# Optimization experiments

Hardware: AMD Instinct MI355X
Metric: run time of the kernel (lower is better)

## Reference

```python
import jax, jax.numpy as jnp
import numpy as np

B, S, H = 8, 1024, 1024
NH, HD = 16, 64  # num heads, head dim


def _split_heads(x):
    # [B,S,H] -> [B,NH,S,HD]
    return x.reshape(B, S, NH, HD).transpose(0, 2, 1, 3)


def setup_inputs() -> dict:
    key = jax.random.key(0)
    ks = jax.random.split(key, 16)
    sc = 1.0 / np.sqrt(H)
    sch = 1.0 / np.sqrt(HD)
    return {
        "hidden_states": jax.random.normal(ks[0], (B, S, H), jnp.float32),
        "attention_mask": jnp.zeros((B, 1, 1, S), jnp.float32),
        "context_embedded": jax.random.normal(ks[1], (B, S, H), jnp.float32),
        "Wq": jax.random.normal(ks[2], (H, H), jnp.float32) * sc,
        "bq": jnp.zeros((H,), jnp.float32),
        "Wk": jax.random.normal(ks[3], (H, H), jnp.float32) * sc,
        "bk": jnp.zeros((H,), jnp.float32),
        "Wv": jax.random.normal(ks[4], (H, H), jnp.float32) * sc,
        "bv": jnp.zeros((H,), jnp.float32),
        "Wcq": jax.random.normal(ks[5], (HD, HD), jnp.float32) * sch,
        "bcq": jnp.zeros((HD,), jnp.float32),
        "Wck": jax.random.normal(ks[6], (HD, HD), jnp.float32) * sch,
        "bck": jnp.zeros((HD,), jnp.float32),
        "w_lqc": jax.random.normal(ks[7], (HD,), jnp.float32) * sch,
        "w_lqq": jax.random.normal(ks[8], (HD,), jnp.float32) * sch,
        "w_lkc": jax.random.normal(ks[9], (HD,), jnp.float32) * sch,
        "w_lkk": jax.random.normal(ks[10], (HD,), jnp.float32) * sch,
    }


def reference(hidden_states, attention_mask, context_embedded,
              Wq, bq, Wk, bk, Wv, bv, Wcq, bcq, Wck, bck,
              w_lqc, w_lqq, w_lkc, w_lkk):
    # projections -> [B,NH,S,HD]
    q = _split_heads(hidden_states @ Wq + bq)
    k = _split_heads(hidden_states @ Wk + bk)
    v = _split_heads(hidden_states @ Wv + bv)
    ce = _split_heads(context_embedded)

    # context gating for queries
    ce_q = ce @ Wcq + bcq
    lam_q = jax.nn.sigmoid(ce_q @ w_lqc[:, None] + q @ w_lqq[:, None])  # [B,NH,S,1]
    q_ctx = (1.0 - lam_q) * q + lam_q * ce_q

    # context gating for keys
    ce_k = ce @ Wck + bck
    lam_k = jax.nn.sigmoid(ce_k @ w_lkc[:, None] + k @ w_lkk[:, None])  # [B,NH,S,1]
    k_ctx = (1.0 - lam_k) * k + lam_k * ce_k

    scores = jnp.einsum("bhqd,bhkd->bhqk", q_ctx, k_ctx) / np.sqrt(HD)
    scores = scores + attention_mask
    probs = jax.nn.softmax(scores, axis=-1)
    ctx = jnp.einsum("bhqk,bhkd->bhqd", probs, v)
    return ctx.transpose(0, 2, 1, 3).reshape(B, S, H)
```

## Files before the change

kernel.cpp:

```cpp
#include <hip/hip_runtime.h>

typedef _Float16 f16;
typedef f16   f16x8 __attribute__((ext_vector_type(8)));
typedef float f32x4 __attribute__((ext_vector_type(4)));

namespace {
constexpr int kB  = 8;
constexpr int kS  = 1024;
constexpr int kH  = 1024;
constexpr int kNH = 16;
constexpr int kHD = 64;
constexpr int kBH = kB * kNH;
constexpr int kRows = kBH * kS;
}

__device__ __forceinline__ void async16(const f16* g, f16* l) {
    __builtin_amdgcn_global_load_lds(
        (const __attribute__((address_space(1))) unsigned int*)g,
        (__attribute__((address_space(3))) unsigned int*)l, 16, 0, 0);
}

__device__ __forceinline__ int phys4(int m, int c) {
    return ((m >> 1) << 3) | ((((m & 1) << 2) | c) ^ ((m >> 1) & 7));
}
__device__ __forceinline__ int phys8(int m, int c) {
    return (m << 3) | (c ^ (m & 7));
}

__global__ __launch_bounds__(256) void cast_inputs_kernel(
    const float* __restrict__ hs, const float* __restrict__ ce,
    f16* __restrict__ hs16, f16* __restrict__ ce16)
{
    int i = (blockIdx.x * 256 + threadIdx.x) * 8;
    const float* src = blockIdx.y ? ce : hs;
    float4 a = *(const float4*)(src + i);
    float4 b = *(const float4*)(src + i + 4);
    union { f16 h[8]; uint4 u; } pk;
    pk.h[0] = (f16)a.x; pk.h[1] = (f16)a.y; pk.h[2] = (f16)a.z; pk.h[3] = (f16)a.w;
    pk.h[4] = (f16)b.x; pk.h[5] = (f16)b.y; pk.h[6] = (f16)b.z; pk.h[7] = (f16)b.w;
    if (blockIdx.y == 0) {
        *(uint4*)(hs16 + i) = pk.u;
    } else {
        int row = i >> 10, col = i & 1023;
        int bb = row >> 10, s = row & 1023;
        int h = col >> 6, d = col & 63;
        size_t o = ((((size_t)(bb * kNH + h) << 10) | s) << 6) | d;
        *(uint4*)(ce16 + o) = pk.u;
    }
}

__global__ __launch_bounds__(256) void transpose_w_kernel(
    const float* __restrict__ Wq, const float* __restrict__ Wk,
    const float* __restrict__ Wv, f16* __restrict__ Wt)
{
    const float* W = (blockIdx.z == 0) ? Wq : (blockIdx.z == 1) ? Wk : Wv;
    f16* out = Wt + (size_t)blockIdx.z * kH * kH;
    __shared__ f16 T[64][72];
    const int tid = threadIdx.x;
    const int k0 = blockIdx.y * 64, n0 = blockIdx.x * 64;
#pragma unroll
    for (int i = 0; i < 4; ++i) {
        int idx = tid + i * 256;
        int r = idx >> 4, cb = (idx & 15) * 4;
        float4 v = *(const float4*)(W + (size_t)(k0 + r) * kH + n0 + cb);
        T[cb + 0][r] = (f16)v.x; T[cb + 1][r] = (f16)v.y;
        T[cb + 2][r] = (f16)v.z; T[cb + 3][r] = (f16)v.w;
    }
    __syncthreads();
#pragma unroll
    for (int i = 0; i < 4; ++i) {
        int idx = tid + i * 256;
        int r = idx >> 4, cb = (idx & 15) * 4;
        union { f16 h[4]; uint2 u; } pk;
#pragma unroll
        for (int j = 0; j < 4; ++j) pk.h[j] = T[r][cb + j];
        *(uint2*)(out + (size_t)(n0 + r) * kH + k0 + cb) = pk.u;
    }
}

__global__ __launch_bounds__(256) void transpose_wc_kernel(
    const float* __restrict__ Wcq, const float* __restrict__ Wck,
    f16* __restrict__ Wct)
{
    const float* W = blockIdx.x ? Wck : Wcq;
    f16* out = Wct + blockIdx.x * kHD * kHD;
    const int t = threadIdx.x;
#pragma unroll
    for (int i = 0; i < 16; ++i) {
        int idx = i * 256 + t;
        int k = idx >> 6, n = idx & 63;
        out[n * 64 + k] = (f16)W[idx];
    }
}

__global__ __launch_bounds__(256) void maskmax_kernel(
    const float* __restrict__ mask, float* __restrict__ mm)
{
    const int b = blockIdx.x, t = threadIdx.x;
    const float* mp = mask + b * kS;
    float v = fmaxf(fmaxf(mp[t], mp[t + 256]), fmaxf(mp[t + 512], mp[t + 768]));
#pragma unroll
    for (int off = 1; off < 64; off <<= 1) v = fmaxf(v, __shfl_xor(v, off, 64));
    __shared__ float red[4];
    if ((t & 63) == 0) red[t >> 6] = v;
    __syncthreads();
    if (t == 0) mm[b] = fmaxf(fmaxf(red[0], red[1]), fmaxf(red[2], red[3]));
}

__global__ __launch_bounds__(256) void qkv_gemm_f16(
    const f16* __restrict__ hs16, const f16* __restrict__ Wt,
    const float* __restrict__ bq, const float* __restrict__ bk,
    const float* __restrict__ bv,
    f16* __restrict__ q16, f16* __restrict__ k16, f16* __restrict__ vt)
{
    const int z = blockIdx.z;
    const f16* Bmat = Wt + (size_t)z * kH * kH;
    const float* bias = (z == 0) ? bq : (z == 1) ? bk : bv;

    __shared__ f16 Atile[128 * 32];
    __shared__ f16 Btile[128 * 32];
    __shared__ f16 Cb[4][64 * 20];

    const int tid = threadIdx.x;
    const int w = tid >> 6, lane = tid & 63;
    const int quad = lane >> 4, mh = lane & 15;
    const int wm = w >> 1, wn = w & 1;
    const int m0 = blockIdx.x * 128, n0 = blockIdx.y * 128;

    const f16* aptr[2]; const f16* bptr[2];
#pragma unroll
    for (int i = 0; i < 2; ++i) {
        int P = (w * 2 + i) * 64 + lane;
        int r2 = P >> 3, s = P & 7;
        int bb = s ^ (r2 & 7);
        int m = (r2 << 1) | (bb >> 2), c = bb & 3;
        aptr[i] = hs16 + (size_t)(m0 + m) * kH + c * 8;
        bptr[i] = Bmat + (size_t)(n0 + m) * kH + c * 8;
    }

    f32x4 acc[4][4];
#pragma unroll
    for (int i = 0; i < 4; ++i)
#pragma unroll
        for (int j = 0; j < 4; ++j) acc[i][j] = (f32x4){0.f, 0.f, 0.f, 0.f};

    int aoff[4], boff[4];
#pragma unroll
    for (int t = 0; t < 4; ++t) {
        aoff[t] = phys4(wm * 64 + t * 16 + mh, quad) * 8;
        boff[t] = phys4(wn * 64 + t * 16 + mh, quad) * 8;
    }

    for (int kt = 0; kt < 32; ++kt) {
        __syncthreads();
        async16(aptr[0], Atile + (w * 2 + 0) * 512);
        async16(aptr[1], Atile + (w * 2 + 1) * 512);
        async16(bptr[0], Btile + (w * 2 + 0) * 512);
        async16(bptr[1], Btile + (w * 2 + 1) * 512);
        aptr[0] += 32; aptr[1] += 32; bptr[0] += 32; bptr[1] += 32;
        __syncthreads();

        f16x8 af[4], bf[4];
#pragma unroll
        for (int t = 0; t < 4; ++t) af[t] = *(const f16x8*)(Atile + aoff[t]);
#pragma unroll
        for (int t = 0; t < 4; ++t) bf[t] = *(const f16x8*)(Btile + boff[t]);
#pragma unroll
        for (int i = 0; i < 4; ++i)
#pragma unroll
            for (int j = 0; j < 4; ++j)
                acc[i][j] = __builtin_amdgcn_mfma_f32_16x16x32_f16(
                    af[i], bf[j], acc[i][j], 0, 0, 0);
    }

    if (z < 2) {
        f16* outp = (z == 0) ? q16 : k16;
        const int h    = (n0 + wn * 64) >> 6;
        const int bbb  = m0 >> 10;
        const int sb   = (m0 & 1023) + wm * 64;
        f16* base = outp + ((size_t)(bbb * kNH + h) * kS + sb) * kHD;
#pragma unroll
        for (int nt = 0; nt < 4; ++nt) {
            const float bn = bias[n0 + wn * 64 + nt * 16 + mh];
#pragma unroll
            for (int mt = 0; mt < 4; ++mt)
#pragma unroll
                for (int r = 0; r < 4; ++r)
                    Cb[w][(mt * 16 + quad * 4 + r) * 20 + mh] =
                        (f16)(acc[mt][nt][r] + bn);
#pragma unroll
            for (int p = 0; p < 4; ++p) {
                int row = (lane >> 2) + p * 16;
                int qtr = lane & 3;
                uint2 v = *(const uint2*)(&Cb[w][row * 20 + qtr * 4]);
                *(uint2*)(base + (size_t)row * kHD + nt * 16 + qtr * 4) = v;
            }
        }
    } else {
#pragma unroll
        for (int nt = 0; nt < 4; ++nt) {
            const int n = n0 + wn * 64 + nt * 16 + mh;
            const int h = n >> 6, d = n & 63;
            const float bn = bias[n];
#pragma unroll
            for (int mt = 0; mt < 4; ++mt) {
                int mbase = m0 + wm * 64 + mt * 16 + quad * 4;
                int bbb = mbase >> 10, s0 = mbase & 1023;
                union { f16 h4[4]; uint2 u; } pk;
#pragma unroll
                for (int r = 0; r < 4; ++r) pk.h4[r] = (f16)(acc[mt][nt][r] + bn);
                *(uint2*)(vt + ((size_t)(bbb * kNH + h) * kHD + d) * kS + s0) = pk.u;
            }
        }
    }
}

__global__ __launch_bounds__(256) void gate_mfma(
    const f16* __restrict__ ce16, const f16* __restrict__ Wct,
    const float* __restrict__ bcq, const float* __restrict__ bck,
    const float* __restrict__ wlqc, const float* __restrict__ wlqq,
    const float* __restrict__ wlkc, const float* __restrict__ wlkk,
    f16* __restrict__ q16, f16* __restrict__ k16,
    unsigned int* __restrict__ kn)
{
    __shared__ f16 Wls[64 * 64];
    __shared__ f16 CeQ[4][64 * 64];
    __shared__ float Tp[4][64 * 17];
    __shared__ float lamS[4][64];

    const int tid = threadIdx.x, w = tid >> 6, lane = tid & 63;
    const int quad = lane >> 4, mh = lane & 15;
    const int gate = blockIdx.x >> 9;
    const int tIdx = (blockIdx.x & 511) * 4 + w;
    const size_t row0 = (size_t)tIdx * 64;

    const float* bc  = gate ? bck  : bcq;
    const float* wlc = gate ? wlkc : wlqc;
    const float* wlx = gate ? wlkk : wlqq;
    f16* xw = (gate ? k16 : q16) + row0 * kHD;
    const f16* cep = ce16 + row0 * kHD;
    const f16* Wcg = Wct + gate * kHD * kHD;

#pragma unroll
    for (int i = 0; i < 2; ++i) {
        int P = tid + i * 256;
        int m = P >> 3, c = P & 7;
        *(uint4*)(Wls + phys8(m, c) * 8) = *(const uint4*)(Wcg + m * 64 + c * 8);
    }
#pragma unroll
    for (int i = 0; i < 8; ++i) {
        int P = i * 64 + lane;
        int m = P >> 3, c = (P & 7) ^ (m & 7);
        async16(cep + m * 64 + c * 8, CeQ[w] + i * 512);
    }
    __syncthreads();

#pragma unroll
    for (int it = 0; it < 8; ++it) {
        int slot = it * 64 + lane;
        int r = slot >> 3, c = slot & 7;
        union { uint4 u; f16 h[8]; } xv;
        xv.u = *(const uint4*)(xw + r * 64 + c * 8);
        float4 wa = ((const float4*)wlx)[c * 2];
        float4 wb = ((const float4*)wlx)[c * 2 + 1];
        float s = (float)xv.h[0] * wa.x + (float)xv.h[1] * wa.y +
                  (float)xv.h[2] * wa.z + (float)xv.h[3] * wa.w +
                  (float)xv.h[4] * wb.x + (float)xv.h[5] * wb.y +
                  (float)xv.h[6] * wb.z + (float)xv.h[7] * wb.w;
        s += __shfl_xor(s, 1, 64);
        s += __shfl_xor(s, 2, 64);
        s += __shfl_xor(s, 4, 64);
        if ((lane & 7) == 0) Tp[w][r * 17 + 16] = s;
    }

    f32x4 acc[4][4];
#pragma unroll
    for (int i = 0; i < 4; ++i)
#pragma unroll
        for (int j = 0; j < 4; ++j) acc[i][j] = (f32x4){0.f, 0.f, 0.f, 0.f};

    f16x8 bfr[4][2];
#pragma unroll
    for (int nt = 0; nt < 4; ++nt)
#pragma unroll
        for (int ks = 0; ks < 2; ++ks)
            bfr[nt][ks] = *(const f16x8*)(Wls + phys8(nt * 16 + mh, ks * 4 + quad) * 8);
#pragma unroll
    for (int mt = 0; mt < 4; ++mt) {
        f16x8 a0 = *(const f16x8*)(CeQ[w] + phys8(mt * 16 + mh, 0 + quad) * 8);
        f16x8 a1 = *(const f16x8*)(CeQ[w] + phys8(mt * 16 + mh, 4 + quad) * 8);
#pragma unroll
        for (int nt = 0; nt < 4; ++nt) {
            acc[mt][nt] = __builtin_amdgcn_mfma_f32_16x16x32_f16(a0, bfr[nt][0], acc[mt][nt], 0, 0, 0);
            acc[mt][nt] = __builtin_amdgcn_mfma_f32_16x16x32_f16(a1, bfr[nt][1], acc[mt][nt], 0, 0, 0);
        }
    }

    float bcv[4], wlcv[4];
#pragma unroll
    for (int nt = 0; nt < 4; ++nt) {
        int n = nt * 16 + mh;
        bcv[nt] = bc[n]; wlcv[nt] = wlc[n];
    }
#pragma unroll
    for (int mt = 0; mt < 4; ++mt) {
#pragma unroll
        for (int r = 0; r < 4; ++r) {
            int m = mt * 16 + quad * 4 + r;
            float tpv = 0.f;
#pragma unroll
            for (int nt = 0; nt < 4; ++nt) {
                float v = acc[mt][nt][r] + bcv[nt];
                int col = nt * 16 + mh;
                CeQ[w][phys8(m, col >> 3) * 8 + (col & 7)] = (f16)v;
                tpv += v * wlcv[nt];
            }
            Tp[w][m * 17 + mh] = tpv;
        }
    }

    float t = 0.f;
#pragma unroll
    for (int j = 0; j < 17; ++j) t += Tp[w][lane * 17 + j];
    lamS[w][lane] = 1.0f / (1.0f + __expf(-t));

    float wmax = 0.f;
#pragma unroll
    for (int it = 0; it < 8; ++it) {
        int slot = it * 64 + lane;
        int r = slot >> 3, c = slot & 7;
        float lam = lamS[w][r];
        union { uint4 u; f16 h[8]; } xv;
        xv.u = *(const uint4*)(xw + r * 64 + c * 8);
        f16x8 cq = *(const f16x8*)(CeQ[w] + phys8(r, c) * 8);
        union { f16 h[8]; uint4 u; } o;
        float ss = 0.f;
#pragma unroll
        for (int j = 0; j < 8; ++j) {
            o.h[j] = (f16)((1.0f - lam) * (float)xv.h[j] + lam * (float)cq[j]);
            float fv = (float)o.h[j];
            ss += fv * fv;
        }
        *(uint4*)(xw + r * 64 + c * 8) = o.u;
        if (gate) {
            ss += __shfl_xor(ss, 1, 64);
            ss += __shfl_xor(ss, 2, 64);
            ss += __shfl_xor(ss, 4, 64);
            wmax = fmaxf(wmax, ss);
        }
    }
    if (gate) {
        wmax = fmaxf(wmax, __shfl_xor(wmax, 8, 64));
        wmax = fmaxf(wmax, __shfl_xor(wmax, 16, 64));
        wmax = fmaxf(wmax, __shfl_xor(wmax, 32, 64));
        if (lane == 0) atomicMax(&kn[tIdx >> 4], __float_as_uint(wmax));
    }
}

__global__ __launch_bounds__(256) void attn_f16(
    const f16* __restrict__ q16, const f16* __restrict__ k16,
    const f16* __restrict__ vt, const float* __restrict__ mask,
    const unsigned int* __restrict__ kn, const float* __restrict__ mm,
    float* __restrict__ out)
{
    __shared__ f16 Ks[2][64 * 64];
    __shared__ f16 Vs[2][64 * 64];
    __shared__ f16 Ps[4][32 * 68];

    const int tid = threadIdx.x;
    const int w = tid >> 6, lane = tid & 63;
    const int quad = lane >> 4, mh = lane & 15;
    const int bh = blockIdx.x, bbb = bh >> 4, h = bh & 15;
    const int q0 = blockIdx.y * 128;
    const float* maskb = mask + bbb * kS;

    int mS[2], cS[2];
#pragma unroll
    for (int i = 0; i < 2; ++i) {
        int P = (w * 2 + i) * 64 + lane;
        mS[i] = P >> 3;
        cS[i] = (P & 7) ^ (mS[i] & 7);
    }
    const f16* kp[2]; const f16* vp[2];
#pragma unroll
    for (int i = 0; i < 2; ++i) {
        kp[i] = k16 + ((size_t)bh * kS + mS[i]) * kHD + cS[i] * 8;
        vp[i] = vt  + ((size_t)bh * kHD + mS[i]) * kS + cS[i] * 8;
    }

    auto issue = [&](f16* Kb, f16* Vb) {
#pragma unroll
        for (int i = 0; i < 2; ++i) {
            async16(kp[i], Kb + (w * 2 + i) * 512);
            async16(vp[i], Vb + (w * 2 + i) * 512);
            kp[i] += 64 * kHD;
            vp[i] += 64;
        }
    };

    issue(Ks[0], Vs[0]);

    f16x8 qf[2][2];
#pragma unroll
    for (int rt = 0; rt < 2; ++rt) {
        const f16* qrow = q16 + ((size_t)bh * kS + q0 + w * 32 + rt * 16 + mh) * kHD;
#pragma unroll
        for (int ks = 0; ks < 2; ++ks) {
            qf[rt][ks] = *(const f16x8*)(qrow + ks * 32 + quad * 8);
#pragma unroll
            for (int j = 0; j < 8; ++j) qf[rt][ks][j] *= (f16)0.125f;
        }
    }

    const float kn2 = __uint_as_float(kn[bh]);
    const float mmb = mm[bbb];
    float bndr[2][4];
#pragma unroll
    for (int rt = 0; rt < 2; ++rt) {
        float qn2 = 0.f;
#pragma unroll
        for (int ks = 0; ks < 2; ++ks)
#pragma unroll
            for (int j = 0; j < 8; ++j) {
                float v = (float)qf[rt][ks][j];
                qn2 += v * v;
            }
        qn2 += __shfl_xor(qn2, 16, 64);
        qn2 += __shfl_xor(qn2, 32, 64);
        const float bnd = sqrtf(qn2 * kn2) + mmb - 9.5f;
#pragma unroll
        for (int r = 0; r < 4; ++r) bndr[rt][r] = __shfl(bnd, quad * 4 + r, 64);
    }

    f32x4 O[2][4];
#pragma unroll
    for (int rt = 0; rt < 2; ++rt)
#pragma unroll
        for (int i = 0; i < 4; ++i) O[rt][i] = (f32x4){0.f, 0.f, 0.f, 0.f};
    float lsum[2][4] = {{0.f, 0.f, 0.f, 0.f}, {0.f, 0.f, 0.f, 0.f}};

    auto step = [&](const f16* Kb, const f16* Vb, int jt) {
        f32x4 S[2][4];
#pragma unroll
        for (int nt = 0; nt < 4; ++nt) {
            f16x8 kf0 = *(const f16x8*)(Kb + phys8(nt * 16 + mh, 0 + quad) * 8);
            f16x8 kf1 = *(const f16x8*)(Kb + phys8(nt * 16 + mh, 4 + quad) * 8);
#pragma unroll
            for (int rt = 0; rt < 2; ++rt) {
                S[rt][nt] = __builtin_amdgcn_mfma_f32_16x16x32_f16(
                    qf[rt][0], kf0, (f32x4){0.f, 0.f, 0.f, 0.f}, 0, 0, 0);
                S[rt][nt] = __builtin_amdgcn_mfma_f32_16x16x32_f16(
                    qf[rt][1], kf1, S[rt][nt], 0, 0, 0);
            }
        }
#pragma unroll
        for (int nt = 0; nt < 4; ++nt) {
            const float mv = maskb[jt + nt * 16 + mh];
#pragma unroll
            for (int rt = 0; rt < 2; ++rt)
#pragma unroll
                for (int r = 0; r < 4; ++r) {
                    float e = __expf(S[rt][nt][r] + mv - bndr[rt][r]);
                    lsum[rt][r] += e;
                    Ps[w][(rt * 16 + quad * 4 + r) * 68 + nt * 16 + mh] = (f16)e;
                }
        }
        f16x8 pf[2][2];
#pragma unroll
        for (int rt = 0; rt < 2; ++rt)
#pragma unroll
            for (int ks = 0; ks < 2; ++ks)
                pf[rt][ks] = *(const f16x8*)(
                    &Ps[w][(rt * 16 + mh) * 68 + ks * 32 + quad * 8]);
#pragma unroll
        for (int dt = 0; dt < 4; ++dt) {
            f16x8 vf0 = *(const f16x8*)(Vb + phys8(dt * 16 + mh, 0 + quad) * 8);
            f16x8 vf1 = *(const f16x8*)(Vb + phys8(dt * 16 + mh, 4 + quad) * 8);
#pragma unroll
            for (int rt = 0; rt < 2; ++rt) {
                O[rt][dt] = __builtin_amdgcn_mfma_f32_16x16x32_f16(
                    pf[rt][0], vf0, O[rt][dt], 0, 0, 0);
                O[rt][dt] = __builtin_amdgcn_mfma_f32_16x16x32_f16(
                    pf[rt][1], vf1, O[rt][dt], 0, 0, 0);
            }
        }
    };

    __syncthreads();

    for (int jt = 0; jt < kS; jt += 128) {
        issue(Ks[1], Vs[1]);
        step(Ks[0], Vs[0], jt);
        __syncthreads();
        if (jt + 128 < kS) issue(Ks[0], Vs[0]);
        step(Ks[1], Vs[1], jt + 64);
        __syncthreads();
    }

#pragma unroll
    for (int rt = 0; rt < 2; ++rt)
#pragma unroll
        for (int r = 0; r < 4; ++r) {
#pragma unroll
            for (int off = 1; off < 16; off <<= 1)
                lsum[rt][r] += __shfl_xor(lsum[rt][r], off, 64);
            lsum[rt][r] = 1.0f / lsum[rt][r];
        }
#pragma unroll
    for (int rt = 0; rt < 2; ++rt)
#pragma unroll
        for (int dt = 0; dt < 4; ++dt)
#pragma unroll
            for (int r = 0; r < 4; ++r) {
                const int s = q0 + w * 32 + rt * 16 + quad * 4 + r;
                out[((size_t)(bbb * kS + s)) * kH + (h << 6) + dt * 16 + mh] =
                    O[rt][dt][r] * lsum[rt][r];
            }
}

extern "C" void kernel_launch(void* const* d_in, const int* in_sizes, int n_in,
                              void* d_out, int out_size, void* d_ws, size_t ws_size,
                              hipStream_t stream) {
    (void)in_sizes; (void)n_in; (void)out_size; (void)ws_size;

    const float* hs   = (const float*)d_in[0];
    const float* mask = (const float*)d_in[1];
    const float* ce   = (const float*)d_in[2];
    const float* Wq   = (const float*)d_in[3];
    const float* bq   = (const float*)d_in[4];
    const float* Wk   = (const float*)d_in[5];
    const float* bk   = (const float*)d_in[6];
    const float* Wv   = (const float*)d_in[7];
    const float* bv   = (const float*)d_in[8];
    const float* Wcq  = (const float*)d_in[9];
    const float* bcq  = (const float*)d_in[10];
    const float* Wck  = (const float*)d_in[11];
    const float* bck  = (const float*)d_in[12];
    const float* wlqc = (const float*)d_in[13];
    const float* wlqq = (const float*)d_in[14];
    const float* wlkc = (const float*)d_in[15];
    const float* wlkk = (const float*)d_in[16];
    float* out = (float*)d_out;

    f16* hs16 = (f16*)d_ws;
    f16* Wt   = hs16 + (size_t)kB * kS * kH;
    f16* q16  = Wt + (size_t)3 * kH * kH;
    f16* k16  = q16 + (size_t)kRows * kHD;
    f16* vt   = k16 + (size_t)kRows * kHD;
    f16* ce16 = vt + (size_t)kRows * kHD;
    f16* Wct  = ce16 + (size_t)kRows * kHD;
    unsigned int* kn = (unsigned int*)(Wct + 2 * kHD * kHD);
    float* mm = (float*)(kn + kBH);

    hipMemsetAsync(kn, 0, kBH * sizeof(unsigned int), stream);

    cast_inputs_kernel<<<dim3(kB * kS * kH / (256 * 8), 2), 256, 0, stream>>>(
        hs, ce, hs16, ce16);
    transpose_w_kernel<<<dim3(16, 16, 3), 256, 0, stream>>>(Wq, Wk, Wv, Wt);
    transpose_wc_kernel<<<dim3(2), 256, 0, stream>>>(Wcq, Wck, Wct);
    maskmax_kernel<<<dim3(kB), 256, 0, stream>>>(mask, mm);

    qkv_gemm_f16<<<dim3(kB * kS / 128, kH / 128, 3), 256, 0, stream>>>(
        hs16, Wt, bq, bk, bv, q16, k16, vt);

    gate_mfma<<<dim3(1024), 256, 0, stream>>>(
        ce16, Wct, bcq, bck, wlqc, wlqq, wlkc, wlkk, q16, k16, kn);

    attn_f16<<<dim3(kBH, kS / 128), 256, 0, stream>>>(
        q16, k16, vt, mask, kn, mm, out);
}
```

Before: 319.4 us.

## Double-buffer QKV GEMM LDS tiles and merge small prep kernels

The QKV GEMM now uses two LDS buffers, so the async global-to-LDS load for the next K tile is issued before the MFMA work on the current tile. This halves the barriers per K step and overlaps memory latency with compute. The epilogue staging buffer reuses the tile LDS to keep the shared-memory footprint in check. Separately, the Wc transpose, the mask-max reduction and the memset of the counter array are merged into one small kernel, which removes two launches and a memset.

```diff
diff --git a/kernel.cpp b/kernel.cpp
--- a/kernel.cpp
+++ b/kernel.cpp
@@ -78,33 +78,34 @@
     }
 }
 
-__global__ __launch_bounds__(256) void transpose_wc_kernel(
+__global__ __launch_bounds__(256) void prep_small_kernel(
     const float* __restrict__ Wcq, const float* __restrict__ Wck,
-    f16* __restrict__ Wct)
+    const float* __restrict__ mask,
+    f16* __restrict__ Wct, unsigned int* __restrict__ kn,
+    float* __restrict__ mm)
 {
-    const float* W = blockIdx.x ? Wck : Wcq;
-    f16* out = Wct + blockIdx.x * kHD * kHD;
     const int t = threadIdx.x;
-#pragma unroll
-    for (int i = 0; i < 16; ++i) {
-        int idx = i * 256 + t;
-        int k = idx >> 6, n = idx & 63;
-        out[n * 64 + k] = (f16)W[idx];
-    }
-}
-
-__global__ __launch_bounds__(256) void maskmax_kernel(
-    const float* __restrict__ mask, float* __restrict__ mm)
-{
-    const int b = blockIdx.x, t = threadIdx.x;
-    const float* mp = mask + b * kS;
-    float v = fmaxf(fmaxf(mp[t], mp[t + 256]), fmaxf(mp[t + 512], mp[t + 768]));
-#pragma unroll
-    for (int off = 1; off < 64; off <<= 1) v = fmaxf(v, __shfl_xor(v, off, 64));
-    __shared__ float red[4];
-    if ((t & 63) == 0) red[t >> 6] = v;
-    __syncthreads();
-    if (t == 0) mm[b] = fmaxf(fmaxf(red[0], red[1]), fmaxf(red[2], red[3]));
+    if (blockIdx.x < 2) {
+        const float* W = blockIdx.x ? Wck : Wcq;
+        f16* out = Wct + blockIdx.x * kHD * kHD;
+#pragma unroll
+        for (int i = 0; i < 16; ++i) {
+            int idx = i * 256 + t;
+            int k = idx >> 6, n = idx & 63;
+            out[n * 64 + k] = (f16)W[idx];
+        }
+        if (blockIdx.x == 0 && t < kBH) kn[t] = 0u;
+    } else {
+        const int b = blockIdx.x - 2;
+        const float* mp = mask + b * kS;
+        float v = fmaxf(fmaxf(mp[t], mp[t + 256]), fmaxf(mp[t + 512], mp[t + 768]));
+#pragma unroll
+        for (int off = 1; off < 64; off <<= 1) v = fmaxf(v, __shfl_xor(v, off, 64));
+        __shared__ float red[4];
+        if ((t & 63) == 0) red[t >> 6] = v;
+        __syncthreads();
+        if (t == 0) mm[b] = fmaxf(fmaxf(red[0], red[1]), fmaxf(red[2], red[3]));
+    }
 }
 
 __global__ __launch_bounds__(256) void qkv_gemm_f16(
@@ -117,9 +118,7 @@
     const f16* Bmat = Wt + (size_t)z * kH * kH;
     const float* bias = (z == 0) ? bq : (z == 1) ? bk : bv;
 
-    __shared__ f16 Atile[128 * 32];
-    __shared__ f16 Btile[128 * 32];
-    __shared__ f16 Cb[4][64 * 20];
+    __shared__ f16 AB[2][2][128 * 32];
 
     const int tid = threadIdx.x;
     const int w = tid >> 6, lane = tid & 63;
@@ -138,6 +137,15 @@
         bptr[i] = Bmat + (size_t)(n0 + m) * kH + c * 8;
     }
 
+    auto issue = [&](int buf) {
+#pragma unroll
+        for (int i = 0; i < 2; ++i) {
+            async16(aptr[i], AB[buf][0] + (w * 2 + i) * 512);
+            async16(bptr[i], AB[buf][1] + (w * 2 + i) * 512);
+            aptr[i] += 32; bptr[i] += 32;
+        }
+    };
+
     f32x4 acc[4][4];
 #pragma unroll
     for (int i = 0; i < 4; ++i)
@@ -151,30 +159,35 @@
         boff[t] = phys4(wn * 64 + t * 16 + mh, quad) * 8;
     }
 
-    for (int kt = 0; kt < 32; ++kt) {
-        __syncthreads();
-        async16(aptr[0], Atile + (w * 2 + 0) * 512);
-        async16(aptr[1], Atile + (w * 2 + 1) * 512);
-        async16(bptr[0], Btile + (w * 2 + 0) * 512);
-        async16(bptr[1], Btile + (w * 2 + 1) * 512);
-        aptr[0] += 32; aptr[1] += 32; bptr[0] += 32; bptr[1] += 32;
-        __syncthreads();
-
+    auto compute = [&](int buf) {
         f16x8 af[4], bf[4];
 #pragma unroll
-        for (int t = 0; t < 4; ++t) af[t] = *(const f16x8*)(Atile + aoff[t]);
-#pragma unroll
-        for (int t = 0; t < 4; ++t) bf[t] = *(const f16x8*)(Btile + boff[t]);
+        for (int t = 0; t < 4; ++t) af[t] = *(const f16x8*)(AB[buf][0] + aoff[t]);
+#pragma unroll
+        for (int t = 0; t < 4; ++t) bf[t] = *(const f16x8*)(AB[buf][1] + boff[t]);
 #pragma unroll
         for (int i = 0; i < 4; ++i)
 #pragma unroll
             for (int j = 0; j < 4; ++j)
                 acc[i][j] = __builtin_amdgcn_mfma_f32_16x16x32_f16(
                     af[i], bf[j], acc[i][j], 0, 0, 0);
+    };
+
+    issue(0);
+    __syncthreads();
+
+    for (int it = 0; it < 16; ++it) {
+        issue(1);
+        compute(0);
+        __syncthreads();
+        if (it < 15) issue(0);
+        compute(1);
+        __syncthreads();
     }
 
     if (z < 2) {
         f16* outp = (z == 0) ? q16 : k16;
+        f16* Cb = &AB[0][0][0] + w * 1280;
         const int h    = (n0 + wn * 64) >> 6;
         const int bbb  = m0 >> 10;
         const int sb   = (m0 & 1023) + wm * 64;
@@ -186,13 +199,13 @@
             for (int mt = 0; mt < 4; ++mt)
 #pragma unroll
                 for (int r = 0; r < 4; ++r)
-                    Cb[w][(mt * 16 + quad * 4 + r) * 20 + mh] =
+                    Cb[(mt * 16 + quad * 4 + r) * 20 + mh] =
                         (f16)(acc[mt][nt][r] + bn);
 #pragma unroll
             for (int p = 0; p < 4; ++p) {
                 int row = (lane >> 2) + p * 16;
                 int qtr = lane & 3;
-                uint2 v = *(const uint2*)(&Cb[w][row * 20 + qtr * 4]);
+                uint2 v = *(const uint2*)(&Cb[row * 20 + qtr * 4]);
                 *(uint2*)(base + (size_t)row * kHD + nt * 16 + qtr * 4) = v;
             }
         }
@@ -552,13 +565,10 @@
     unsigned int* kn = (unsigned int*)(Wct + 2 * kHD * kHD);
     float* mm = (float*)(kn + kBH);
 
-    hipMemsetAsync(kn, 0, kBH * sizeof(unsigned int), stream);
-
     cast_inputs_kernel<<<dim3(kB * kS * kH / (256 * 8), 2), 256, 0, stream>>>(
         hs, ce, hs16, ce16);
     transpose_w_kernel<<<dim3(16, 16, 3), 256, 0, stream>>>(Wq, Wk, Wv, Wt);
-    transpose_wc_kernel<<<dim3(2), 256, 0, stream>>>(Wcq, Wck, Wct);
-    maskmax_kernel<<<dim3(kB), 256, 0, stream>>>(mask, mm);
+    prep_small_kernel<<<dim3(10), 256, 0, stream>>>(Wcq, Wck, mask, Wct, kn, mm);
 
     qkv_gemm_f16<<<dim3(kB * kS / 128, kH / 128, 3), 256, 0, stream>>>(
         hs16, Wt, bq, bk, bv, q16, k16, vt);
```

Result: faster. 310.7 us (-2.7%).
